# Optimization experiments

Measured on AMD Instinct MI355X. Metric: run time of the kernel, lower is better.

## Reference

```python
import jax, jax.numpy as jnp
import numpy as np

C = 384       # in_channels
P = 64        # patch_size (H = W = P)
NH = 3        # num_heads
EPS = 1e-5
SCALE = (C // NH) ** -0.5  # head_dim in torch code = in_channels // num_heads


def _ln(x, w, b):
    m = jnp.mean(x, axis=-1, keepdims=True)
    v = jnp.var(x, axis=-1, keepdims=True)
    return (x - m) / jnp.sqrt(v + EPS) * w + b


def _dwt2d(x):
    # Haar DWT, x: [B, C, H, W] -> [B, 4C, H/2, W/2] channels = [LL, HL, LH, HH]
    x01 = x[:, :, 0::2, :] / 2
    x02 = x[:, :, 1::2, :] / 2
    x1 = x01[:, :, :, 0::2]
    x2 = x02[:, :, :, 0::2]
    x3 = x01[:, :, :, 1::2]
    x4 = x02[:, :, :, 1::2]
    return jnp.concatenate(
        [x1 + x2 + x3 + x4, -x1 - x2 + x3 + x4, -x1 + x2 - x3 + x4, x1 - x2 - x3 + x4],
        axis=1)


def _iwt2d(x):
    # inverse Haar, x: [B, 4C, h, w] -> [B, C, 2h, 2w]
    B, C4, h, w = x.shape
    c = C4 // 4
    x1 = x[:, 0:c] / 2
    x2 = x[:, c:2 * c] / 2
    x3 = x[:, 2 * c:3 * c] / 2
    x4 = x[:, 3 * c:4 * c] / 2
    out = jnp.zeros((B, c, h * 2, w * 2), x.dtype)
    out = out.at[:, :, 0::2, 0::2].set(x1 - x2 - x3 + x4)
    out = out.at[:, :, 1::2, 0::2].set(x1 - x2 + x3 - x4)
    out = out.at[:, :, 0::2, 1::2].set(x1 + x2 - x3 - x4)
    out = out.at[:, :, 1::2, 1::2].set(x1 + x2 + x3 + x4)
    return out


def setup_inputs():
    key = jax.random.key(0)
    ks = jax.random.split(key, 6)
    B, L = 8, P * P
    s = 0.02
    f32 = jnp.float32
    return {
        "sf": jax.random.normal(ks[0], (B, L, C), f32),
        "wf": jax.random.normal(ks[1], (B, L, C), f32),
        "q_w": jax.random.normal(ks[2], (C, C), f32) * s,
        "q_b": jnp.zeros((C,), f32),
        "q_ln_w": jnp.ones((C,), f32),
        "q_ln_b": jnp.zeros((C,), f32),
        "kv_w": jax.random.normal(ks[3], (2 * C, C), f32) * s,
        "kv_b": jnp.zeros((2 * C,), f32),
        "kv_ln_w": jnp.ones((2 * C,), f32),
        "kv_ln_b": jnp.zeros((2 * C,), f32),
        "out_w": jax.random.normal(ks[4], (C, C), f32) * s,
        "out_b": jnp.zeros((C,), f32),
    }


def reference(sf, wf, q_w, q_b, q_ln_w, q_ln_b, kv_w, kv_b, kv_ln_w, kv_ln_b, out_w, out_b):
    B, L, _ = sf.shape
    H = W = P
    h, w = H // 2, W // 2
    n = h * w  # L // 4

    t_sf = _ln(sf @ q_w.T + q_b, q_ln_w, q_ln_b)            # [B, L, C]
    t_wf = _ln(wf @ kv_w.T + kv_b, kv_ln_w, kv_ln_b)        # [B, L, 2C]

    t_sf = t_sf.reshape(B, H, W, C).transpose(0, 3, 1, 2)
    t_wf = t_wf.reshape(B, H, W, 2 * C).transpose(0, 3, 1, 2)

    t_sf = _dwt2d(t_sf).transpose(0, 2, 3, 1).reshape(B, n, 4 * C)
    t_wf = _dwt2d(t_wf).transpose(0, 2, 3, 1).reshape(B, n, 8 * C)

    k_all, v_all = jnp.split(t_wf, 2, axis=-1)              # each [B, n, 4C]
    q1, q2 = t_sf[..., :C], t_sf[..., C:]
    k1, k2 = k_all[..., :C], k_all[..., C:]
    v1, v2 = v_all[..., :C], v_all[..., C:]

    # branch 1: full single-head attention on LL sub-band (no scale, as in source)
    att1 = jax.nn.softmax(jnp.einsum('bnc,bmc->bnm', q1, k1), axis=-1)
    x1 = jnp.einsum('bnm,bmc->bnc', att1, v1)
    x1 = x1.reshape(B, h, w, C).transpose(0, 3, 1, 2)       # [B, C, h, w]

    # branch 2: multi-head attention on high-freq sub-bands, per-head dim = 3C/NH = C
    d = (3 * C) // NH
    q2 = q2.reshape(B, n, NH, d).transpose(0, 2, 1, 3)      # [B, NH, n, d]
    k2 = k2.reshape(B, n, NH, d).transpose(0, 2, 1, 3)
    v2 = v2.reshape(B, n, NH, d).transpose(0, 2, 3, 1)      # [B, NH, d, n]
    att2 = jax.nn.softmax(jnp.einsum('bhnd,bhmd->bhnm', q2, k2) * SCALE, axis=-1)
    x2 = jnp.einsum('bhdm,bhmn->bhdn', v2, att2)            # [B, NH, d, n]
    x2 = x2.reshape(B, NH * d, h, w)                        # [B, 3C, h, w]

    x = jnp.concatenate([x1, x2], axis=1)                   # [B, 4C, h, w]
    x = _iwt2d(x)                                           # [B, C, H, W]
    x = x.transpose(0, 2, 3, 1).reshape(B, L, C)
    return x @ out_w.T + out_b
```

## Files before the change

kernel.cpp:

```cpp
#include <hip/hip_runtime.h>
#include <hip/hip_bf16.h>

typedef unsigned short u16;
typedef unsigned int u32;
typedef __attribute__((ext_vector_type(8))) short short8;
typedef __attribute__((ext_vector_type(4))) float f32x4;

#define MFMA_BF16(A, B, C) __builtin_amdgcn_mfma_f32_16x16x32_bf16(A, B, C, 0, 0, 0)

#define SCALE2 0.08838834764831845f
#define LNEPS 1e-5f

__device__ __forceinline__ float b2f(u16 u) {
  return __uint_as_float(((u32)u) << 16);
}
__device__ __forceinline__ u16 f2b(float f) {
  u32 x = __float_as_uint(f);
  return (u16)((x + 0x7fffu + ((x >> 16) & 1u)) >> 16);
}
__device__ __forceinline__ float ldf(const float* p) { return *p; }
__device__ __forceinline__ float ldf(const u16* p) { return b2f(*p); }
__device__ __forceinline__ void stf(float* p, float v) { *p = v; }
__device__ __forceinline__ void stf(u16* p, float v) { *p = f2b(v); }

template <int SPLIT, typename TX, typename TO>
__global__ __launch_bounds__(256) void gemm_mfma(
    const TX* __restrict__ X, const float* __restrict__ W,
    const float* __restrict__ bias, TO* __restrict__ out) {
  __shared__ __align__(16) u16 AH[128 * 40];
  __shared__ __align__(16) u16 BH[128 * 40];
  __shared__ __align__(16) u16 AL[SPLIT ? 128 * 40 : 8];
  __shared__ __align__(16) u16 BL[SPLIT ? 128 * 40 : 8];
  const int tid = threadIdx.x;
  const int w = tid >> 6, lane = tid & 63;
  const int t = lane & 15, qd = lane >> 4;
  const int wm = w & 1, wn = w >> 1;
  const int m0 = blockIdx.y * 128, n0 = blockIdx.x * 128;
  f32x4 acc[4][4];
#pragma unroll
  for (int i = 0; i < 4; ++i)
#pragma unroll
    for (int j = 0; j < 4; ++j) acc[i][j] = (f32x4){0.f, 0.f, 0.f, 0.f};
  for (int kt = 0; kt < 384; kt += 32) {
#pragma unroll
    for (int rep = 0; rep < 4; ++rep) {
      int e = tid + rep * 256;
      int m = e >> 3, k4 = (e & 7) * 4;
      if constexpr (sizeof(TX) == 4) {
        float4 v = *(const float4*)(X + (size_t)(m0 + m) * 384 + kt + k4);
        u16 h0 = f2b(v.x), h1 = f2b(v.y), h2 = f2b(v.z), h3 = f2b(v.w);
        u32 hp0 = (u32)h0 | ((u32)h1 << 16), hp1 = (u32)h2 | ((u32)h3 << 16);
        *(uint2*)&AH[m * 40 + k4] = make_uint2(hp0, hp1);
        if (SPLIT) {
          u16 l0 = f2b(v.x - b2f(h0)), l1 = f2b(v.y - b2f(h1));
          u16 l2 = f2b(v.z - b2f(h2)), l3 = f2b(v.w - b2f(h3));
          *(uint2*)&AL[m * 40 + k4] =
              make_uint2((u32)l0 | ((u32)l1 << 16), (u32)l2 | ((u32)l3 << 16));
        }
      } else {
        uint2 raw = *(const uint2*)(X + (size_t)(m0 + m) * 384 + kt + k4);
        *(uint2*)&AH[m * 40 + k4] = raw;
      }
      float4 wv = *(const float4*)(W + (size_t)(n0 + m) * 384 + kt + k4);
      u16 wh0 = f2b(wv.x), wh1 = f2b(wv.y), wh2 = f2b(wv.z), wh3 = f2b(wv.w);
      *(uint2*)&BH[m * 40 + k4] =
          make_uint2((u32)wh0 | ((u32)wh1 << 16), (u32)wh2 | ((u32)wh3 << 16));
      if (SPLIT) {
        u16 wl0 = f2b(wv.x - b2f(wh0)), wl1 = f2b(wv.y - b2f(wh1));
        u16 wl2 = f2b(wv.z - b2f(wh2)), wl3 = f2b(wv.w - b2f(wh3));
        *(uint2*)&BL[m * 40 + k4] =
            make_uint2((u32)wl0 | ((u32)wl1 << 16), (u32)wl2 | ((u32)wl3 << 16));
      }
    }
    __syncthreads();
    short8 af[4], bf[4], al[4], bl[4];
#pragma unroll
    for (int mi = 0; mi < 4; ++mi) {
      af[mi] = *(const short8*)&AH[(wm * 64 + mi * 16 + t) * 40 + qd * 8];
      bf[mi] = *(const short8*)&BH[(wn * 64 + mi * 16 + t) * 40 + qd * 8];
      if (SPLIT) {
        al[mi] = *(const short8*)&AL[(wm * 64 + mi * 16 + t) * 40 + qd * 8];
        bl[mi] = *(const short8*)&BL[(wn * 64 + mi * 16 + t) * 40 + qd * 8];
      }
    }
#pragma unroll
    for (int mi = 0; mi < 4; ++mi)
#pragma unroll
      for (int ni = 0; ni < 4; ++ni) {
        acc[mi][ni] = MFMA_BF16(af[mi], bf[ni], acc[mi][ni]);
        if (SPLIT) {
          acc[mi][ni] = MFMA_BF16(al[mi], bf[ni], acc[mi][ni]);
          acc[mi][ni] = MFMA_BF16(af[mi], bl[ni], acc[mi][ni]);
        }
      }
    __syncthreads();
  }
#pragma unroll
  for (int ni = 0; ni < 4; ++ni) {
    int n = n0 + wn * 64 + ni * 16 + t;
    float bv = bias[n];
#pragma unroll
    for (int mi = 0; mi < 4; ++mi)
#pragma unroll
      for (int r = 0; r < 4; ++r) {
        int m = m0 + wm * 64 + mi * 16 + qd * 4 + r;
        stf(&out[(size_t)m * 384 + n], acc[mi][ni][r] + bv);
      }
  }
}

template <typename T>
__global__ __launch_bounds__(256) void ln_inplace(
    T* __restrict__ Tb, const float* __restrict__ w, const float* __restrict__ b, int N) {
  const int row = blockIdx.x, tid = threadIdx.x;
  T* Tr = Tb + (size_t)row * N;
  float vals[3];
  float s = 0.f, ss = 0.f;
  int nv = 0;
  for (int i = tid; i < N; i += 256) {
    float v = ldf(&Tr[i]);
    vals[nv++] = v;
    s += v; ss += v * v;
  }
#pragma unroll
  for (int mk = 32; mk; mk >>= 1) { s += __shfl_xor(s, mk); ss += __shfl_xor(ss, mk); }
  __shared__ float red[8];
  if ((tid & 63) == 0) { red[tid >> 6] = s; red[4 + (tid >> 6)] = ss; }
  __syncthreads();
  s = red[0] + red[1] + red[2] + red[3];
  ss = red[4] + red[5] + red[6] + red[7];
  float inv = 1.f / (float)N;
  float mean = s * inv;
  float var = fmaxf(ss * inv - mean * mean, 0.f);
  float rstd = rsqrtf(var + LNEPS);
  nv = 0;
  for (int i = tid; i < N; i += 256) {
    float v = (vals[nv++] - mean) * rstd * w[i] + b[i];
    stf(&Tr[i], v);
  }
}

__global__ __launch_bounds__(256) void ln_wf_split(
    float* __restrict__ lo, u16* __restrict__ hi,
    const float* __restrict__ w, const float* __restrict__ b) {
  const int row = blockIdx.x, tid = threadIdx.x;
  float* L = lo + (size_t)row * 384;
  u16* H = hi + (size_t)row * 384;
  float vals[3];
  float s = 0.f, ss = 0.f;
  int nv = 0;
  for (int i = tid; i < 768; i += 256) {
    float v = (i < 384) ? L[i] : b2f(H[i - 384]);
    vals[nv++] = v;
    s += v; ss += v * v;
  }
#pragma unroll
  for (int mk = 32; mk; mk >>= 1) { s += __shfl_xor(s, mk); ss += __shfl_xor(ss, mk); }
  __shared__ float red[8];
  if ((tid & 63) == 0) { red[tid >> 6] = s; red[4 + (tid >> 6)] = ss; }
  __syncthreads();
  s = red[0] + red[1] + red[2] + red[3];
  ss = red[4] + red[5] + red[6] + red[7];
  float mean = s * (1.f / 768.f);
  float var = fmaxf(ss * (1.f / 768.f) - mean * mean, 0.f);
  float rstd = rsqrtf(var + LNEPS);
  nv = 0;
  for (int i = 0 + tid; i < 768; i += 256) {
    float v = (vals[nv++] - mean) * rstd * w[i] + b[i];
    if (i < 384) L[i] = v; else H[i - 384] = f2b(v);
  }
}

__global__ __launch_bounds__(256) void dwt_sf(
    const float* __restrict__ T, u16* __restrict__ q1h, u16* __restrict__ q1l,
    u16* __restrict__ q2) {
  const int blk = blockIdx.x;
  const int b = blk >> 10, pos = blk & 1023;
  const int i = pos >> 5, j = pos & 31;
  const int p00 = (i * 2) * 64 + j * 2;
  const float* base = T + (size_t)b * 4096 * 384;
  for (int ch = threadIdx.x; ch < 384; ch += 256) {
    float a  = base[(size_t)p00 * 384 + ch];
    float cc = base[(size_t)(p00 + 1) * 384 + ch];
    float bb = base[(size_t)(p00 + 64) * 384 + ch];
    float dd = base[(size_t)(p00 + 65) * 384 + ch];
    float s0 = 0.5f * ( a + bb + cc + dd);
    float s1 = 0.5f * (-a - bb + cc + dd);
    float s2 = 0.5f * (-a + bb - cc + dd);
    float s3 = 0.5f * ( a - bb - cc + dd);
    size_t po = (size_t)(b * 1024 + pos) * 384 + ch;
    u16 h = f2b(s0);
    q1h[po] = h;
    q1l[po] = f2b(s0 - b2f(h));
    q2[(size_t)((b * 3 + 0) * 1024 + pos) * 384 + ch] = f2b(s1);
    q2[(size_t)((b * 3 + 1) * 1024 + pos) * 384 + ch] = f2b(s2);
    q2[(size_t)((b * 3 + 2) * 1024 + pos) * 384 + ch] = f2b(s3);
  }
}

__global__ __launch_bounds__(256) void dwt_wf_split(
    const float* __restrict__ lo, const u16* __restrict__ hi,
    u16* __restrict__ k1h, u16* __restrict__ k1l, u16* __restrict__ v1,
    u16* __restrict__ k2, u16* __restrict__ v2) {
  const int blk = blockIdx.x;
  const int b = blk >> 10, pos = blk & 1023;
  const int i = pos >> 5, j = pos & 31;
  const int p00 = (i * 2) * 64 + j * 2;
  for (int ch = threadIdx.x; ch < 768; ch += 256) {
    float a, bb, cc, dd;
    if (ch < 384) {
      const float* base = lo + (size_t)b * 4096 * 384;
      a  = base[(size_t)p00 * 384 + ch];
      cc = base[(size_t)(p00 + 1) * 384 + ch];
      bb = base[(size_t)(p00 + 64) * 384 + ch];
      dd = base[(size_t)(p00 + 65) * 384 + ch];
    } else {
      const u16* base = hi + (size_t)b * 4096 * 384;
      int c = ch - 384;
      a  = b2f(base[(size_t)p00 * 384 + c]);
      cc = b2f(base[(size_t)(p00 + 1) * 384 + c]);
      bb = b2f(base[(size_t)(p00 + 64) * 384 + c]);
      dd = b2f(base[(size_t)(p00 + 65) * 384 + c]);
    }
    float s0 = 0.5f * ( a + bb + cc + dd);
    float s1 = 0.5f * (-a - bb + cc + dd);
    float s2 = 0.5f * (-a + bb - cc + dd);
    float s3 = 0.5f * ( a - bb - cc + dd);
    if (ch < 384) {
      size_t po = (size_t)(b * 1024 + pos) * 384 + ch;
      u16 h = f2b(s0);
      k1h[po] = h;
      k1l[po] = f2b(s0 - b2f(h));
      v1[po] = f2b(s2);
      k2[(size_t)((b * 3 + 1) * 1024 + pos) * 384 + ch] = f2b(s1);
      v2[(size_t)((b * 3 + 1) * 1024 + pos) * 384 + ch] = f2b(s3);
    } else {
      int c = ch - 384;
      k2[(size_t)((b * 3 + 0) * 1024 + pos) * 384 + c] = f2b(s0);
      k2[(size_t)((b * 3 + 2) * 1024 + pos) * 384 + c] = f2b(s1);
      v2[(size_t)((b * 3 + 0) * 1024 + pos) * 384 + c] = f2b(s2);
      v2[(size_t)((b * 3 + 2) * 1024 + pos) * 384 + c] = f2b(s3);
    }
  }
}

__global__ __launch_bounds__(256) void transpose_rm(
    const u16* __restrict__ in, u16* __restrict__ out) {
  __shared__ u16 T[64][65];
  const int tid = threadIdx.x;
  const int bh = blockIdx.z, r0 = blockIdx.y * 64, c0 = blockIdx.x * 64;
  const u16* ip = in + ((size_t)bh * 1024 + r0) * 384 + c0;
  for (int i = tid; i < 2048; i += 256) {
    int r = i >> 5, c2 = i & 31;
    u32 v = *(const u32*)(ip + (size_t)r * 384 + c2 * 2);
    T[c2 * 2][r] = (u16)v;
    T[c2 * 2 + 1][r] = (u16)(v >> 16);
  }
  __syncthreads();
  u16* op = out + ((size_t)bh * 384 + c0) * 1024 + r0;
  for (int i = tid; i < 2048; i += 256) {
    int c = i >> 5, r2 = i & 31;
    u32 v = (u32)T[c][r2 * 2] | ((u32)T[c][r2 * 2 + 1] << 16);
    *(u32*)(op + (size_t)c * 1024 + r2 * 2) = v;
  }
}

__device__ __forceinline__ void xcd24v2(int L, int& bh, int& o0) {
  int s = L >> 3;
  bh = (s >> 4) * 8 + (L & 7);
  o0 = (s & 15) * 64;
}

__global__ __launch_bounds__(256) void att2_stats(
    const u16* __restrict__ q, const u16* __restrict__ k,
    float2* __restrict__ stats, float scale) {
  __shared__ __align__(16) u16 S[2][12 * 32 * 40];
  const int tid = threadIdx.x, w = tid >> 6, lane = tid & 63;
  const int t = lane & 15, qd = lane >> 4;
  int bh, o0;
  xcd24v2(blockIdx.x, bh, o0);
  short8 Ah[12];
  {
    const u16* qp = q + ((size_t)bh * 1024 + o0 + w * 16 + t) * 384 + qd * 8;
#pragma unroll
    for (int ks = 0; ks < 12; ++ks) Ah[ks] = *(const short8*)(qp + ks * 32);
  }
  float m[4] = {-1e30f, -1e30f, -1e30f, -1e30f}, l[4] = {0.f, 0.f, 0.f, 0.f};
  const u16* kb = k + (size_t)bh * 1024 * 384;
  int buf = 0;
  for (int st = 0; st < 32; ++st) {
#pragma unroll
    for (int i = 0; i < 6; ++i) {
      int u = tid + i * 256;
      int r = u / 48, c8 = u % 48;
      int ks = c8 >> 2, qq = c8 & 3;
      uint4 v = *(const uint4*)(kb + (size_t)(st * 32 + r) * 384 + c8 * 8);
      *(uint4*)&S[buf][(ks * 32 + r) * 40 + qq * 8] = v;
    }
    __syncthreads();
    f32x4 Sa0 = {0.f,0.f,0.f,0.f}, Sb0 = {0.f,0.f,0.f,0.f};
    f32x4 Sa1 = {0.f,0.f,0.f,0.f}, Sb1 = {0.f,0.f,0.f,0.f};
#pragma unroll
    for (int ks = 0; ks < 12; ks += 2) {
      short8 B00 = *(const short8*)&S[buf][(ks * 32 + t) * 40 + qd * 8];
      short8 B01 = *(const short8*)&S[buf][((ks + 1) * 32 + t) * 40 + qd * 8];
      short8 B10 = *(const short8*)&S[buf][(ks * 32 + 16 + t) * 40 + qd * 8];
      short8 B11 = *(const short8*)&S[buf][((ks + 1) * 32 + 16 + t) * 40 + qd * 8];
      Sa0 = MFMA_BF16(Ah[ks], B00, Sa0);
      Sb0 = MFMA_BF16(Ah[ks + 1], B01, Sb0);
      Sa1 = MFMA_BF16(Ah[ks], B10, Sa1);
      Sb1 = MFMA_BF16(Ah[ks + 1], B11, Sb1);
    }
#pragma unroll
    for (int r = 0; r < 4; ++r) {
      float s0 = (Sa0[r] + Sb0[r]) * scale;
      float s1 = (Sa1[r] + Sb1[r]) * scale;
      float mx = fmaxf(s0, s1);
#pragma unroll
      for (int mk = 1; mk < 16; mk <<= 1) mx = fmaxf(mx, __shfl_xor(mx, mk));
      float nm = fmaxf(m[r], mx);
      float e = __expf(s0 - nm) + __expf(s1 - nm);
#pragma unroll
      for (int mk = 1; mk < 16; mk <<= 1) e += __shfl_xor(e, mk);
      l[r] = l[r] * __expf(m[r] - nm) + e;
      m[r] = nm;
    }
    buf ^= 1;
  }
  if (t == 0) {
#pragma unroll
    for (int r = 0; r < 4; ++r)
      stats[(size_t)bh * 1024 + o0 + w * 16 + qd * 4 + r] =
          make_float2(m[r], 1.f / l[r]);
  }
}

__global__ __launch_bounds__(256, 2) void att2_accum(
    const u16* __restrict__ own, const u16* __restrict__ str,
    const u16* __restrict__ vt, const float2* __restrict__ stats,
    u16* __restrict__ xall, float scale) {
  __shared__ __align__(16) u16 SQ[12 * 32 * 40];
  __shared__ __align__(16) u16 SV[24 * 16 * 40];
  __shared__ __align__(16) u16 P[4][16 * 40];
  const int tid = threadIdx.x, w = tid >> 6, lane = tid & 63;
  const int t = lane & 15, qd = lane >> 4;
  int bh, o0;
  xcd24v2(blockIdx.x, bh, o0);
  short8 Ah[12];
  {
    const u16* op = own + ((size_t)bh * 1024 + o0 + w * 16 + t) * 384 + qd * 8;
#pragma unroll
    for (int ks = 0; ks < 12; ++ks) Ah[ks] = *(const short8*)(op + ks * 32);
  }
  f32x4 acc[24];
#pragma unroll
  for (int i = 0; i < 24; ++i) acc[i] = (f32x4){0.f, 0.f, 0.f, 0.f};
  const u16* sb = str + (size_t)bh * 1024 * 384;
  const u16* vb = vt + (size_t)bh * 384 * 1024;
  u16* Pw = &P[w][0];
  for (int st = 0; st < 32; ++st) {
    __syncthreads();
#pragma unroll
    for (int i = 0; i < 6; ++i) {
      int u = tid + i * 256;
      int r = u / 48, c8 = u % 48;
      int ks = c8 >> 2, qq = c8 & 3;
      uint4 v = *(const uint4*)(sb + (size_t)(st * 32 + r) * 384 + c8 * 8);
      *(uint4*)&SQ[(ks * 32 + r) * 40 + qq * 8] = v;
    }
#pragma unroll
    for (int i = 0; i < 6; ++i) {
      int u = tid + i * 256;
      int d = u >> 2, cq = u & 3;
      uint4 v = *(const uint4*)(vb + (size_t)d * 1024 + st * 32 + cq * 8);
      *(uint4*)&SV[d * 40 + cq * 8] = v;
    }
    float2 cs0 = stats[(size_t)bh * 1024 + st * 32 + t];
    float2 cs1 = stats[(size_t)bh * 1024 + st * 32 + 16 + t];
    __syncthreads();
    f32x4 Sa0 = {0.f,0.f,0.f,0.f}, Sb0 = {0.f,0.f,0.f,0.f};
    f32x4 Sa1 = {0.f,0.f,0.f,0.f}, Sb1 = {0.f,0.f,0.f,0.f};
#pragma unroll
    for (int ks = 0; ks < 12; ks += 2) {
      short8 B00 = *(const short8*)&SQ[(ks * 32 + t) * 40 + qd * 8];
      short8 B01 = *(const short8*)&SQ[((ks + 1) * 32 + t) * 40 + qd * 8];
      short8 B10 = *(const short8*)&SQ[(ks * 32 + 16 + t) * 40 + qd * 8];
      short8 B11 = *(const short8*)&SQ[((ks + 1) * 32 + 16 + t) * 40 + qd * 8];
      Sa0 = MFMA_BF16(Ah[ks], B00, Sa0);
      Sb0 = MFMA_BF16(Ah[ks + 1], B01, Sb0);
      Sa1 = MFMA_BF16(Ah[ks], B10, Sa1);
      Sb1 = MFMA_BF16(Ah[ks + 1], B11, Sb1);
    }
#pragma unroll
    for (int r = 0; r < 4; ++r) {
      float p0 = __expf((Sa0[r] + Sb0[r]) * scale - cs0.x) * cs0.y;
      float p1 = __expf((Sa1[r] + Sb1[r]) * scale - cs1.x) * cs1.y;
      Pw[(qd * 4 + r) * 40 + t] = f2b(p0);
      Pw[(qd * 4 + r) * 40 + 16 + t] = f2b(p1);
    }
    short8 Pa = *(const short8*)&Pw[t * 40 + qd * 8];
#pragma unroll
    for (int nj = 0; nj < 24; ++nj) {
      short8 Vf = *(const short8*)&SV[(nj * 16 + t) * 40 + qd * 8];
      acc[nj] = MFMA_BF16(Pa, Vf, acc[nj]);
    }
  }
  const int b_out = bh / 3, off = (1 + bh % 3) * 384;
#pragma unroll
  for (int nj = 0; nj < 24; ++nj)
#pragma unroll
    for (int r = 0; r < 4; ++r) {
      int row = o0 + w * 16 + qd * 4 + r;
      int d = nj * 16 + t;
      xall[((size_t)b_out * 1024 + row) * 1536 + off + d] = f2b(acc[nj][r]);
    }
}

__global__ __launch_bounds__(256, 2) void att1_fused(
    const u16* __restrict__ qh, const u16* __restrict__ ql,
    const u16* __restrict__ kh, const u16* __restrict__ kl,
    const u16* __restrict__ vt, u16* __restrict__ xall) {
  __shared__ __align__(16) u16 KH[12 * 32 * 40];
  __shared__ __align__(16) u16 KL[12 * 32 * 40];
  __shared__ __align__(16) u16 P[2][16 * 40];
  __shared__ float2 comb[2][2][16];
  const int tid = threadIdx.x, w = tid >> 6, lane = tid & 63;
  const int t = lane & 15, qd = lane >> 4;
  const int wr = w & 1, sh = w >> 1;
  const int bh = blockIdx.x & 7, o0 = (blockIdx.x >> 3) * 32;
  short8 Ah[12], Al[12];
  {
    const u16* qp  = qh + ((size_t)bh * 1024 + o0 + wr * 16 + t) * 384 + qd * 8;
    const u16* qp2 = ql + ((size_t)bh * 1024 + o0 + wr * 16 + t) * 384 + qd * 8;
#pragma unroll
    for (int ks = 0; ks < 12; ++ks) {
      Ah[ks] = *(const short8*)(qp + ks * 32);
      Al[ks] = *(const short8*)(qp2 + ks * 32);
    }
  }
  f32x4 acc[12];
#pragma unroll
  for (int i = 0; i < 12; ++i) acc[i] = (f32x4){0.f, 0.f, 0.f, 0.f};
  float m[4] = {-1e30f, -1e30f, -1e30f, -1e30f}, l[4] = {0.f, 0.f, 0.f, 0.f};
  const u16* khb = kh + (size_t)bh * 1024 * 384;
  const u16* klb = kl + (size_t)bh * 1024 * 384;
  const u16* vbase = vt + ((size_t)bh * 384 + sh * 192 + t) * 1024;
#pragma unroll
  for (int i = 0; i < 6; ++i) {
    int u = tid + i * 256;
    int r = u / 48, c8 = u % 48;
    int ks = c8 >> 2, j8 = c8 & 3;
    *(uint4*)&KH[(ks * 32 + r) * 40 + j8 * 8] =
        *(const uint4*)(khb + (size_t)r * 384 + c8 * 8);
    *(uint4*)&KL[(ks * 32 + r) * 40 + j8 * 8] =
        *(const uint4*)(klb + (size_t)r * 384 + c8 * 8);
  }
  __syncthreads();
  for (int st = 0; st < 32; ++st) {
    short8 Vr[12];
#pragma unroll
    for (int nj = 0; nj < 12; ++nj)
      Vr[nj] = *(const short8*)(vbase + (size_t)nj * 16 * 1024 + st * 32 + qd * 8);
    f32x4 Shh = {0.f,0.f,0.f,0.f}, Slh = {0.f,0.f,0.f,0.f}, Shl = {0.f,0.f,0.f,0.f};
#pragma unroll
    for (int ks = 0; ks < 12; ++ks) {
      short8 Bh = *(const short8*)&KH[(ks * 32 + sh * 16 + t) * 40 + qd * 8];
      short8 Bl = *(const short8*)&KL[(ks * 32 + sh * 16 + t) * 40 + qd * 8];
      Shh = MFMA_BF16(Ah[ks], Bh, Shh);
      Slh = MFMA_BF16(Al[ks], Bh, Slh);
      Shl = MFMA_BF16(Ah[ks], Bl, Shl);
    }
    float s[4], mx[4], e[4];
#pragma unroll
    for (int r = 0; r < 4; ++r) {
      s[r] = Shh[r] + Slh[r] + Shl[r];
      float v = s[r];
#pragma unroll
      for (int mk = 1; mk < 16; mk <<= 1) v = fmaxf(v, __shfl_xor(v, mk));
      mx[r] = v;
      float ee = __expf(s[r] - v);
#pragma unroll
      for (int mk = 1; mk < 16; mk <<= 1) ee += __shfl_xor(ee, mk);
      e[r] = ee;
    }
    if (t == 0) {
#pragma unroll
      for (int r = 0; r < 4; ++r)
        comb[wr][sh][qd * 4 + r] = make_float2(mx[r], e[r]);
    }
    __syncthreads();
    if (st < 31) {
#pragma unroll
      for (int i = 0; i < 6; ++i) {
        int u = tid + i * 256;
        int r = u / 48, c8 = u % 48;
        int ks = c8 >> 2, j8 = c8 & 3;
        *(uint4*)&KH[(ks * 32 + r) * 40 + j8 * 8] =
            *(const uint4*)(khb + (size_t)((st + 1) * 32 + r) * 384 + c8 * 8);
        *(uint4*)&KL[(ks * 32 + r) * 40 + j8 * 8] =
            *(const uint4*)(klb + (size_t)((st + 1) * 32 + r) * 384 + c8 * 8);
      }
    }
#pragma unroll
    for (int r = 0; r < 4; ++r) {
      float2 c0 = comb[wr][0][qd * 4 + r];
      float2 c1 = comb[wr][1][qd * 4 + r];
      float nm = fmaxf(m[r], fmaxf(c0.x, c1.x));
      float sc = __expf(m[r] - nm);
      l[r] = l[r] * sc + c0.y * __expf(c0.x - nm) + c1.y * __expf(c1.x - nm);
      m[r] = nm;
#pragma unroll
      for (int nj = 0; nj < 12; ++nj) acc[nj][r] *= sc;
      P[wr][(qd * 4 + r) * 40 + sh * 16 + t] = f2b(__expf(s[r] - nm));
    }
    __syncthreads();
    short8 Pa = *(const short8*)&P[wr][t * 40 + qd * 8];
#pragma unroll
    for (int nj = 0; nj < 12; ++nj) acc[nj] = MFMA_BF16(Pa, Vr[nj], acc[nj]);
  }
#pragma unroll
  for (int r = 0; r < 4; ++r) {
    float inv = 1.f / l[r];
    int row = o0 + wr * 16 + qd * 4 + r;
#pragma unroll
    for (int nj = 0; nj < 12; ++nj) {
      int d = sh * 192 + nj * 16 + t;
      xall[((size_t)bh * 1024 + row) * 1536 + d] = f2b(acc[nj][r] * inv);
    }
  }
}

__global__ __launch_bounds__(256) void iwt_y(const u16* __restrict__ xall, u16* __restrict__ y) {
  const int blk = blockIdx.x;
  const int b = blk >> 10, pos = blk & 1023;
  const int i = pos >> 5, j = pos & 31;
  const u16* xr = xall + (size_t)(b * 1024 + pos) * 1536;
  u16* yb = y + (size_t)b * 4096 * 384;
  const int p00 = (i * 2) * 64 + j * 2;
  for (int c = threadIdx.x; c < 384; c += 256) {
    float g1 = 0.5f * b2f(xr[c]);
    float g2 = 0.5f * b2f(xr[c + 384]);
    float g3 = 0.5f * b2f(xr[c + 768]);
    float g4 = 0.5f * b2f(xr[c + 1152]);
    yb[(size_t)p00 * 384 + c]        = f2b(g1 - g2 - g3 + g4);
    yb[(size_t)(p00 + 64) * 384 + c] = f2b(g1 - g2 + g3 - g4);
    yb[(size_t)(p00 + 1) * 384 + c]  = f2b(g1 + g2 - g3 - g4);
    yb[(size_t)(p00 + 65) * 384 + c] = f2b(g1 + g2 + g3 + g4);
  }
}

extern "C" void kernel_launch(void* const* d_in, const int* in_sizes, int n_in,
                              void* d_out, int out_size, void* d_ws, size_t ws_size,
                              hipStream_t stream) {
  (void)in_sizes; (void)n_in; (void)out_size; (void)ws_size;
  const float* sf      = (const float*)d_in[0];
  const float* wf      = (const float*)d_in[1];
  const float* q_w     = (const float*)d_in[2];
  const float* q_b     = (const float*)d_in[3];
  const float* q_ln_w  = (const float*)d_in[4];
  const float* q_ln_b  = (const float*)d_in[5];
  const float* kv_w    = (const float*)d_in[6];
  const float* kv_b    = (const float*)d_in[7];
  const float* kv_ln_w = (const float*)d_in[8];
  const float* kv_ln_b = (const float*)d_in[9];
  const float* out_w   = (const float*)d_in[10];
  const float* out_b   = (const float*)d_in[11];
  float* out = (float*)d_out;

  char* p = (char*)d_ws;
  float* A  = (float*)p; p += 50331648;
  float* B1 = (float*)p; p += 50331648;
  u16*   B2 = (u16*)p;   p += 25165824;
  u16* q1h = (u16*)p; p += 6291456;
  u16* q1l = (u16*)p; p += 6291456;
  u16* q2  = (u16*)p; p += 18874368;
  u16* v2  = (u16*)p; p += 18874368;
  float2* stats1 = (float2*)p; p += 65536;
  float2* stats2 = (float2*)p;
  (void)stats1;
  u16* k1h = (u16*)A;
  u16* k1l = k1h + 3145728;
  u16* v1  = k1l + 3145728;
  u16* k2  = v1 + 3145728;
  u16* v1t = k2 + 9437184;
  u16* xall = (u16*)B1;
  u16* v2t = B2;
  u16* y   = B2;

  gemm_mfma<1, float, float><<<dim3(3, 256), 256, 0, stream>>>(sf, q_w, q_b, A);
  ln_inplace<float><<<32768, 256, 0, stream>>>(A, q_ln_w, q_ln_b, 384);
  gemm_mfma<1, float, float><<<dim3(3, 256), 256, 0, stream>>>(wf, kv_w, kv_b, B1);
  gemm_mfma<0, float, u16><<<dim3(3, 256), 256, 0, stream>>>(wf, kv_w + 384 * 384, kv_b + 384, B2);
  ln_wf_split<<<32768, 256, 0, stream>>>(B1, B2, kv_ln_w, kv_ln_b);

  dwt_sf<<<8192, 256, 0, stream>>>(A, q1h, q1l, q2);
  dwt_wf_split<<<8192, 256, 0, stream>>>(B1, B2, k1h, k1l, v1, k2, v2);

  transpose_rm<<<dim3(6, 16, 8), 256, 0, stream>>>(v1, v1t);
  transpose_rm<<<dim3(6, 16, 24), 256, 0, stream>>>(v2, v2t);

  att2_stats<<<384, 256, 0, stream>>>(q2, k2, stats2, SCALE2);
  att1_fused<<<256, 256, 0, stream>>>(q1h, q1l, k1h, k1l, v1t, xall);
  att2_accum<<<384, 256, 0, stream>>>(k2, q2, v2t, stats2, xall, SCALE2);

  iwt_y<<<8192, 256, 0, stream>>>(xall, y);
  gemm_mfma<0, u16, float><<<dim3(3, 256), 256, 0, stream>>>(y, out_w, out_b, out);
}
```

Measured before the change: 811.4 us.

## Split att1 key sequence into two segments with separate merge kernel

The LL-band attention kernel now splits the 1024 keys into two halves, so the grid doubles from 256 to 512 blocks, and each block writes unnormalized fp32 partial outputs plus running max and sum. A new merge kernel combines the two partials using log-sum-exp rescaling and writes bf16 into xall. The K shared-memory tile stride is also changed to 1288 per k-slice, likely to reduce bank conflicts. The aim is better CU occupancy on a 256-block launch, at the cost of extra fp32 partial traffic and one more kernel launch.

```diff
diff --git a/kernel.cpp b/kernel.cpp
--- a/kernel.cpp
+++ b/kernel.cpp
@@ -419,15 +419,20 @@
 __global__ __launch_bounds__(256, 2) void att1_fused(
     const u16* __restrict__ qh, const u16* __restrict__ ql,
     const u16* __restrict__ kh, const u16* __restrict__ kl,
-    const u16* __restrict__ vt, u16* __restrict__ xall) {
-  __shared__ __align__(16) u16 KH[12 * 32 * 40];
-  __shared__ __align__(16) u16 KL[12 * 32 * 40];
+    const u16* __restrict__ vt, float* __restrict__ part,
+    float2* __restrict__ ml) {
+  __shared__ __align__(16) u16 KH[12 * 1288];
+  __shared__ __align__(16) u16 KL[12 * 1288];
   __shared__ __align__(16) u16 P[2][16 * 40];
   __shared__ float2 comb[2][2][16];
   const int tid = threadIdx.x, w = tid >> 6, lane = tid & 63;
   const int t = lane & 15, qd = lane >> 4;
   const int wr = w & 1, sh = w >> 1;
-  const int bh = blockIdx.x & 7, o0 = (blockIdx.x >> 3) * 32;
+  const int bh = blockIdx.x & 7;
+  const int q = blockIdx.x >> 3;
+  const int o0 = (q & 31) * 32;
+  const int sseg = q >> 5;
+  const int sbase = sseg * 512;
   short8 Ah[12], Al[12];
   {
     const u16* qp  = qh + ((size_t)bh * 1024 + o0 + wr * 16 + t) * 384 + qd * 8;
@@ -444,19 +449,19 @@
   float m[4] = {-1e30f, -1e30f, -1e30f, -1e30f}, l[4] = {0.f, 0.f, 0.f, 0.f};
   const u16* khb = kh + (size_t)bh * 1024 * 384;
   const u16* klb = kl + (size_t)bh * 1024 * 384;
-  const u16* vbase = vt + ((size_t)bh * 384 + sh * 192 + t) * 1024;
+  const u16* vbase = vt + ((size_t)bh * 384 + sh * 192 + t) * 1024 + sbase;
 #pragma unroll
   for (int i = 0; i < 6; ++i) {
     int u = tid + i * 256;
     int r = u / 48, c8 = u % 48;
     int ks = c8 >> 2, j8 = c8 & 3;
-    *(uint4*)&KH[(ks * 32 + r) * 40 + j8 * 8] =
-        *(const uint4*)(khb + (size_t)r * 384 + c8 * 8);
-    *(uint4*)&KL[(ks * 32 + r) * 40 + j8 * 8] =
-        *(const uint4*)(klb + (size_t)r * 384 + c8 * 8);
+    *(uint4*)&KH[ks * 1288 + r * 40 + j8 * 8] =
+        *(const uint4*)(khb + (size_t)(sbase + r) * 384 + c8 * 8);
+    *(uint4*)&KL[ks * 1288 + r * 40 + j8 * 8] =
+        *(const uint4*)(klb + (size_t)(sbase + r) * 384 + c8 * 8);
   }
   __syncthreads();
-  for (int st = 0; st < 32; ++st) {
+  for (int st = 0; st < 16; ++st) {
     short8 Vr[12];
 #pragma unroll
     for (int nj = 0; nj < 12; ++nj)
@@ -464,8 +469,8 @@
     f32x4 Shh = {0.f,0.f,0.f,0.f}, Slh = {0.f,0.f,0.f,0.f}, Shl = {0.f,0.f,0.f,0.f};
 #pragma unroll
     for (int ks = 0; ks < 12; ++ks) {
-      short8 Bh = *(const short8*)&KH[(ks * 32 + sh * 16 + t) * 40 + qd * 8];
-      short8 Bl = *(const short8*)&KL[(ks * 32 + sh * 16 + t) * 40 + qd * 8];
+      short8 Bh = *(const short8*)&KH[ks * 1288 + (sh * 16 + t) * 40 + qd * 8];
+      short8 Bl = *(const short8*)&KL[ks * 1288 + (sh * 16 + t) * 40 + qd * 8];
       Shh = MFMA_BF16(Ah[ks], Bh, Shh);
       Slh = MFMA_BF16(Al[ks], Bh, Slh);
       Shl = MFMA_BF16(Ah[ks], Bl, Shl);
@@ -489,16 +494,16 @@
         comb[wr][sh][qd * 4 + r] = make_float2(mx[r], e[r]);
     }
     __syncthreads();
-    if (st < 31) {
+    if (st < 15) {
 #pragma unroll
       for (int i = 0; i < 6; ++i) {
         int u = tid + i * 256;
         int r = u / 48, c8 = u % 48;
         int ks = c8 >> 2, j8 = c8 & 3;
-        *(uint4*)&KH[(ks * 32 + r) * 40 + j8 * 8] =
-            *(const uint4*)(khb + (size_t)((st + 1) * 32 + r) * 384 + c8 * 8);
-        *(uint4*)&KL[(ks * 32 + r) * 40 + j8 * 8] =
-            *(const uint4*)(klb + (size_t)((st + 1) * 32 + r) * 384 + c8 * 8);
+        *(uint4*)&KH[ks * 1288 + r * 40 + j8 * 8] =
+            *(const uint4*)(khb + (size_t)(sbase + (st + 1) * 32 + r) * 384 + c8 * 8);
+        *(uint4*)&KL[ks * 1288 + r * 40 + j8 * 8] =
+            *(const uint4*)(klb + (size_t)(sbase + (st + 1) * 32 + r) * 384 + c8 * 8);
       }
     }
 #pragma unroll
@@ -518,16 +523,36 @@
 #pragma unroll
     for (int nj = 0; nj < 12; ++nj) acc[nj] = MFMA_BF16(Pa, Vr[nj], acc[nj]);
   }
+  float* pb = part + ((size_t)(sseg * 8 + bh) * 1024 + o0 + wr * 16) * 384;
 #pragma unroll
   for (int r = 0; r < 4; ++r) {
-    float inv = 1.f / l[r];
-    int row = o0 + wr * 16 + qd * 4 + r;
-#pragma unroll
-    for (int nj = 0; nj < 12; ++nj) {
-      int d = sh * 192 + nj * 16 + t;
-      xall[((size_t)bh * 1024 + row) * 1536 + d] = f2b(acc[nj][r] * inv);
-    }
-  }
+    int row = qd * 4 + r;
+#pragma unroll
+    for (int nj = 0; nj < 12; ++nj)
+      pb[(size_t)row * 384 + sh * 192 + nj * 16 + t] = acc[nj][r];
+  }
+  if (sh == 0 && t == 0) {
+#pragma unroll
+    for (int r = 0; r < 4; ++r)
+      ml[sseg * 8192 + bh * 1024 + o0 + wr * 16 + qd * 4 + r] =
+          make_float2(m[r], l[r]);
+  }
+}
+
+__global__ __launch_bounds__(192) void att1_merge(
+    const float* __restrict__ part, const float2* __restrict__ ml,
+    u16* __restrict__ xall) {
+  const int rb = blockIdx.x;
+  float2 a = ml[rb];
+  float2 b = ml[8192 + rb];
+  float M = fmaxf(a.x, b.x);
+  float e0 = __expf(a.x - M), e1 = __expf(b.x - M);
+  float inv = 1.f / (a.y * e0 + b.y * e1);
+  const float* p0 = part + (size_t)rb * 384;
+  const float* p1 = part + (size_t)(8192 + rb) * 384;
+  u16* xr = xall + (size_t)rb * 1536;
+  for (int ch = threadIdx.x; ch < 384; ch += 192)
+    xr[ch] = f2b((p0[ch] * e0 + p1[ch] * e1) * inv);
 }
 
 __global__ __launch_bounds__(256) void iwt_y(const u16* __restrict__ xall, u16* __restrict__ y) {
@@ -583,7 +608,9 @@
   u16* v1  = k1l + 3145728;
   u16* k2  = v1 + 3145728;
   u16* v1t = k2 + 9437184;
+  float2* ml1 = (float2*)((char*)A + 44040192);
   u16* xall = (u16*)B1;
+  float* part1 = (float*)((char*)B1 + 25165824);
   u16* v2t = B2;
   u16* y   = B2;
 
@@ -600,7 +627,8 @@
   transpose_rm<<<dim3(6, 16, 24), 256, 0, stream>>>(v2, v2t);
 
   att2_stats<<<384, 256, 0, stream>>>(q2, k2, stats2, SCALE2);
-  att1_fused<<<256, 256, 0, stream>>>(q1h, q1l, k1h, k1l, v1t, xall);
+  att1_fused<<<512, 256, 0, stream>>>(q1h, q1l, k1h, k1l, v1t, part1, ml1);
+  att1_merge<<<8192, 192, 0, stream>>>(part1, ml1, xall);
   att2_accum<<<384, 256, 0, stream>>>(k2, q2, v2t, stats2, xall, SCALE2);
 
   iwt_y<<<8192, 256, 0, stream>>>(xall, y);
```

After: 762.2 us. 6.1% less time.
